# Performance work log

Measured on AMD Instinct MI355X. Metric: run time of the kernel, lower is better.

Reference implementation:

```python
import jax, jax.numpy as jnp
import numpy as np

V, E, H = 32000, 512, 1024  # vocab, embed_dim, hidden_dim
N, T = 32, 256              # batch, seq_len


def setup_inputs() -> dict:
    key = jax.random.key(0)
    ks = jax.random.split(key, 8)
    s = 1.0 / np.sqrt(H)
    return {
        "words": jax.random.randint(ks[0], (N, T), 0, V),
        "hidden_state": jnp.zeros((N, H), jnp.float32),
        "embed_w": jax.random.uniform(ks[1], (V, E), minval=-1.0, maxval=1.0) * 0.1,
        "w_ih": jax.random.uniform(ks[2], (3 * H, E), minval=-s, maxval=s),
        "w_hh": jax.random.uniform(ks[3], (3 * H, H), minval=-s, maxval=s),
        "b_ih": jax.random.uniform(ks[4], (3 * H,), minval=-s, maxval=s),
        "b_hh": jax.random.uniform(ks[5], (3 * H,), minval=-s, maxval=s),
        "emit_w": jax.random.uniform(ks[6], (V, H), minval=-s, maxval=s),
        "emit_b": jnp.zeros((V,), jnp.float32),
    }


def reference(words, hidden_state, embed_w, w_ih, w_hh, b_ih, b_hh, emit_w, emit_b):
    n = words.shape[0]
    emb = embed_w[words]                      # [N, T, E]
    xs = (jnp.swapaxes(emb[:, :-1], 0, 1),    # [T-1, N, E] inputs x_{t-1}
          jnp.swapaxes(words[:, 1:], 0, 1))   # [T-1, N]    targets w_t

    def gru_cell(x, h):
        gi = x @ w_ih.T + b_ih                # [N, 3H]
        gh = h @ w_hh.T + b_hh                # [N, 3H]
        i_r, i_z, i_n = jnp.split(gi, 3, axis=-1)
        h_r, h_z, h_n = jnp.split(gh, 3, axis=-1)
        r = jax.nn.sigmoid(i_r + h_r)
        z = jax.nn.sigmoid(i_z + h_z)
        nn_ = jnp.tanh(i_n + r * h_n)
        return (1.0 - z) * nn_ + z * h

    def step(carry, inp):
        h, acc = carry
        x, w = inp
        h = gru_cell(x, h)
        logits = h @ emit_w.T + emit_b        # [N, V]
        logp = jax.nn.log_softmax(logits, axis=-1)
        ll = jnp.take_along_axis(logp, w[:, None], axis=1)[:, 0]  # [N]
        return (h, acc + ll), None

    acc0 = jnp.zeros((n,), hidden_state.dtype)
    (h_final, word_marginals), _ = jax.lax.scan(step, (hidden_state, acc0), xs)
    return word_marginals, h_final
```

## Files before the change

kernel.cpp:

```cpp
#include <hip/hip_runtime.h>
#include <cstdint>

#define V_    32000
#define E_    512
#define H_    1024
#define N_    32
#define T_    256
#define TS    255
#define NWG_B 64
#define CB_   250
#define RB_   64
#define MROW  8192
#define GI_CB 24

typedef _Float16 f16;
typedef _Float16 half8 __attribute__((ext_vector_type(8)));
typedef float floatx4 __attribute__((ext_vector_type(4)));
typedef unsigned long long u64;


__global__ void prep_emit16(const float* __restrict__ emit_w, f16* __restrict__ out) {
  const int64_t nchunk = (int64_t)V_ * H_ / 8;
  int64_t i = (int64_t)blockIdx.x * blockDim.x + threadIdx.x;
  for (; i < nchunk; i += (int64_t)gridDim.x * blockDim.x) {
    const float4* src = (const float4*)(emit_w + i * 8);
    float4 a = src[0], b = src[1];
    half8 h;
    h[0] = (f16)a.x; h[1] = (f16)a.y; h[2] = (f16)a.z; h[3] = (f16)a.w;
    h[4] = (f16)b.x; h[5] = (f16)b.y; h[6] = (f16)b.z; h[7] = (f16)b.w;
    *(half8*)(out + i * 8) = h;
  }
}

__global__ void prep_whh(const float* __restrict__ w_hh, f16* __restrict__ whh) {
  int idx = blockIdx.x * blockDim.x + threadIdx.x;
  if (idx >= 192 * 32 * 64) return;
  int lane = idx & 63;
  int kt   = (idx >> 6) & 31;
  int jt   = (idx >> 6) >> 5;
  int col  = jt * 16 + (lane & 15);
  int k0   = kt * 32 + (lane >> 4) * 8;
  const float* src = w_hh + (int64_t)col * H_ + k0;
  half8 h;
#pragma unroll
  for (int i = 0; i < 8; ++i) h[i] = (f16)src[i];
  *(half8*)(whh + (int64_t)idx * 8) = h;
}

__global__ void prep_wih16(const float* __restrict__ w_ih, f16* __restrict__ out) {
  int idx = blockIdx.x * blockDim.x + threadIdx.x;
  if (idx >= 3072 * 512 / 8) return;
  const float4* src = (const float4*)(w_ih + (int64_t)idx * 8);
  float4 a = src[0], b = src[1];
  half8 h;
  h[0] = (f16)a.x; h[1] = (f16)a.y; h[2] = (f16)a.z; h[3] = (f16)a.w;
  h[4] = (f16)b.x; h[5] = (f16)b.y; h[6] = (f16)b.z; h[7] = (f16)b.w;
  *(half8*)(out + (int64_t)idx * 8) = h;
}

__global__ void prep_xemb(const int* __restrict__ words, const float* __restrict__ embed_w,
                          f16* __restrict__ xemb) {
  int idx = blockIdx.x * blockDim.x + threadIdx.x;
  if (idx >= TS * N_ * (E_ / 8)) return;
  int u = idx & 63;
  int n = (idx >> 6) & 31;
  int t = idx >> 11;
  int word = words[n * T_ + t];
  const float* src = embed_w + (int64_t)word * E_ + u * 8;
  half8 h;
#pragma unroll
  for (int i = 0; i < 8; ++i) h[i] = (f16)src[i];
  *(half8*)(xemb + (int64_t)(t * N_ + n) * E_ + u * 8) = h;
}

__global__ void prep_init(const float* __restrict__ h0, f16* __restrict__ xh,
                          unsigned* __restrict__ slots) {
  int idx = blockIdx.x * blockDim.x + threadIdx.x;
  if (idx < N_ * H_) {
    f16 v = (f16)h0[idx];
    xh[idx] = v;
    xh[N_ * H_ + idx] = v;
  }
  if (idx < 1024) slots[idx] = 0;
}


#define LDK 72

__launch_bounds__(256, 2)
__global__ void gi_gemm(const f16* __restrict__ xemb, const f16* __restrict__ wih16,
                        f16* __restrict__ gi2) {
  const int cb = blockIdx.x % GI_CB;
  const int rb = blockIdx.x / GI_CB;
  const int tid = threadIdx.x;
  const int w = tid >> 6, lane = tid & 63;
  const int wm = w & 1, wn = w >> 1;
  const int l15 = lane & 15, l4 = lane >> 4;

  __shared__ f16 lA[128 * LDK];
  __shared__ f16 lB[128 * LDK];

  floatx4 acc[4][4];
#pragma unroll
  for (int mt = 0; mt < 4; ++mt)
#pragma unroll
    for (int nt = 0; nt < 4; ++nt) { acc[mt][nt][0] = 0.f; acc[mt][nt][1] = 0.f; acc[mt][nt][2] = 0.f; acc[mt][nt][3] = 0.f; }

  const f16* gA = xemb + (int64_t)rb * 128 * E_;
  const f16* gB = wih16 + (int64_t)cb * 128 * E_;

  for (int kb = 0; kb < 8; ++kb) {
    __syncthreads();
#pragma unroll
    for (int i = 0; i < 4; ++i) {
      int idx = i * 256 + tid;
      int row = idx >> 3, u = idx & 7;
      int64_t goff = (int64_t)row * E_ + kb * 64 + u * 8;
      *(half8*)(lA + row * LDK + u * 8) = *(const half8*)(gA + goff);
      *(half8*)(lB + row * LDK + u * 8) = *(const half8*)(gB + goff);
    }
    __syncthreads();
#pragma unroll
    for (int ks = 0; ks < 2; ++ks) {
      half8 af[4], bf[4];
#pragma unroll
      for (int mt = 0; mt < 4; ++mt)
        af[mt] = *(const half8*)(lA + (wm * 64 + mt * 16 + l15) * LDK + ks * 32 + l4 * 8);
#pragma unroll
      for (int nt = 0; nt < 4; ++nt)
        bf[nt] = *(const half8*)(lB + (wn * 64 + nt * 16 + l15) * LDK + ks * 32 + l4 * 8);
#pragma unroll
      for (int mt = 0; mt < 4; ++mt)
#pragma unroll
        for (int nt = 0; nt < 4; ++nt)
          acc[mt][nt] = __builtin_amdgcn_mfma_f32_16x16x32_f16(af[mt], bf[nt], acc[mt][nt], 0, 0, 0);
    }
  }

#pragma unroll
  for (int mt = 0; mt < 4; ++mt) {
#pragma unroll
    for (int r = 0; r < 4; ++r) {
      int g = rb * 128 + wm * 64 + mt * 16 + l4 * 4 + r;
      if (g < TS * N_) {
        int tt = g >> 5, n = g & 31;
        f16* gb = gi2 + ((int64_t)tt * 3072 + cb * 128 + wn * 64) * 32 + n;
#pragma unroll
        for (int nt = 0; nt < 4; ++nt)
          gb[(nt * 16 + l15) * 32] = (f16)acc[mt][nt][r];
      }
    }
  }
}


__device__ inline u64 aload64(const void* p) {
  return __hip_atomic_load((const u64*)p, __ATOMIC_RELAXED, __HIP_MEMORY_SCOPE_AGENT);
}
__device__ inline unsigned aload32(const void* p) {
  return __hip_atomic_load((const unsigned*)p, __ATOMIC_RELAXED, __HIP_MEMORY_SCOPE_AGENT);
}

__device__ inline void gbar3(unsigned* slots, unsigned tval, int b) {
  __syncthreads();
  if (threadIdx.x == 0) {
    __builtin_amdgcn_s_waitcnt(0);
    __hip_atomic_store(slots + b * 16, tval, __ATOMIC_RELAXED, __HIP_MEMORY_SCOPE_AGENT);
  }
  if (threadIdx.x < 64) {
    unsigned* my = slots + threadIdx.x * 16;
    while (__hip_atomic_load(my, __ATOMIC_RELAXED, __HIP_MEMORY_SCOPE_AGENT) < tval)
      __builtin_amdgcn_s_sleep(1);
  }
  __syncthreads();
}

__launch_bounds__(512, 1)
__global__ void phaseB(const f16* __restrict__ whh, const f16* __restrict__ gi2,
                       f16* __restrict__ xh, const float* __restrict__ b_ih,
                       const float* __restrict__ b_hh, f16* __restrict__ hall,
                       float* __restrict__ out, unsigned* __restrict__ slots) {
  const int b = blockIdx.x;
  const int tid = threadIdx.x;
  const int w = tid >> 6;
  const int lane = tid & 63;
  const int l15 = lane & 15, l4 = lane >> 4;

  __shared__ float part[8][32][49];

  const int n_g = tid & 31;
  const int jl = tid >> 5;
  const int j = b * 16 + jl;
  const float biasr = b_ih[j] + b_hh[j];
  const float biasz = b_ih[H_ + j] + b_hh[H_ + j];
  const float bihn = b_ih[2 * H_ + j];
  const float bhhn = b_hh[2 * H_ + j];

  half8 wf[3][4];
#pragma unroll
  for (int g = 0; g < 3; ++g) {
    int jt = g * 64 + b;
#pragma unroll
    for (int k = 0; k < 4; ++k)
      wf[g][k] = *(const half8*)(whh + (((int64_t)jt * 32 + (w * 4 + k)) * 64 + lane) * 8);
  }

  for (int t = 0; t < TS; ++t) {
    const f16* xh_rd = xh + (t & 1) * (N_ * H_);
    f16* xh_wr = xh + ((t + 1) & 1) * (N_ * H_);

    const f16* gbase = gi2 + (int64_t)t * 3072 * 32 + n_g;
    float gvr = (float)gbase[(int64_t)j * 32];
    float gvz = (float)gbase[(int64_t)(H_ + j) * 32];
    float gvn = (float)gbase[(int64_t)(2 * H_ + j) * 32];
    unsigned hraw = aload32(xh_rd + n_g * H_ + (j & ~1));
    unsigned short hbits = (jl & 1) ? (unsigned short)(hraw >> 16) : (unsigned short)(hraw & 0xffffu);
    float hold = (float)__builtin_bit_cast(f16, hbits);

    floatx4 acc[3][2];
#pragma unroll
    for (int g = 0; g < 3; ++g)
#pragma unroll
      for (int m = 0; m < 2; ++m) { acc[g][m][0] = 0.f; acc[g][m][1] = 0.f; acc[g][m][2] = 0.f; acc[g][m][3] = 0.f; }

    half8 a0[4], a1[4];
#pragma unroll
    for (int k = 0; k < 4; ++k) {
      const f16* base = xh_rd + (w * 4 + k) * 32 + l4 * 8;
      union { half8 h; u64 u[2]; } x0, x1;
      const u64* p0 = (const u64*)(base + (int64_t)l15 * H_);
      const u64* p1 = (const u64*)(base + (int64_t)(l15 + 16) * H_);
      x0.u[0] = aload64(p0); x0.u[1] = aload64(p0 + 1);
      x1.u[0] = aload64(p1); x1.u[1] = aload64(p1 + 1);
      a0[k] = x0.h; a1[k] = x1.h;
    }
#pragma unroll
    for (int k = 0; k < 4; ++k) {
#pragma unroll
      for (int g = 0; g < 3; ++g) {
        acc[g][0] = __builtin_amdgcn_mfma_f32_16x16x32_f16(a0[k], wf[g][k], acc[g][0], 0, 0, 0);
        acc[g][1] = __builtin_amdgcn_mfma_f32_16x16x32_f16(a1[k], wf[g][k], acc[g][1], 0, 0, 0);
      }
    }

#pragma unroll
    for (int g = 0; g < 3; ++g)
#pragma unroll
      for (int m = 0; m < 2; ++m)
#pragma unroll
        for (int r = 0; r < 4; ++r)
          part[w][m * 16 + l4 * 4 + r][g * 16 + l15] = acc[g][m][r];
    __syncthreads();

    float gr = biasr + gvr, gz = biasz + gvz, gin = bihn + gvn, ghn = bhhn;
#pragma unroll
    for (int ww = 0; ww < 8; ++ww) {
      gr += part[ww][n_g][jl];
      gz += part[ww][n_g][16 + jl];
      ghn += part[ww][n_g][32 + jl];
    }
    float rg = 1.f / (1.f + __expf(-gr));
    float zg = 1.f / (1.f + __expf(-gz));
    float nn = tanhf(gin + rg * ghn);
    float hnew = (1.f - zg) * nn + zg * hold;

    unsigned short hb = __builtin_bit_cast(unsigned short, (f16)hnew);
    unsigned other = (unsigned)__shfl_xor((int)(unsigned)hb, 32, 64);
    if (!(jl & 1)) {
      unsigned packed = (unsigned)hb | (other << 16);
      __hip_atomic_store((unsigned*)(xh_wr + n_g * H_ + j), packed,
                         __ATOMIC_RELAXED, __HIP_MEMORY_SCOPE_AGENT);
      *(unsigned*)(hall + ((int64_t)t * N_ + n_g) * H_ + j) = packed;
    }
    if (t == TS - 1) out[32 + n_g * H_ + j] = hnew;

    if (t < TS - 1) gbar3(slots, (unsigned)(t + 1), b);
  }
}


__device__ inline void gload_lds16(const f16* g, f16* l) {
  __builtin_amdgcn_global_load_lds((const __attribute__((address_space(1))) void*)g,
                                   (__attribute__((address_space(3))) void*)l, 16, 0, 0);
}

__launch_bounds__(256, 2)
__global__ void phaseC(const f16* __restrict__ hall, const f16* __restrict__ emit16,
                       const float* __restrict__ emit_b, float* __restrict__ spart) {
  const int wgid = (blockIdx.x & 7) * 2000 + (blockIdx.x >> 3);
  const int cb = wgid >> 6;
  const int rb = wgid & 63;
  const int tid = threadIdx.x;
  const int w = tid >> 6, lane = tid & 63;
  const int wm = w & 1, wn = w >> 1;
  const int l15 = lane & 15, l4 = lane >> 4;

  __shared__ f16 lA[128 * 64];
  __shared__ f16 lB[128 * 64];
  __shared__ float rs[2][128];

  floatx4 acc[4][4];
#pragma unroll
  for (int mt = 0; mt < 4; ++mt)
#pragma unroll
    for (int nt = 0; nt < 4; ++nt) { acc[mt][nt][0] = 0.f; acc[mt][nt][1] = 0.f; acc[mt][nt][2] = 0.f; acc[mt][nt][3] = 0.f; }

  const f16* gA = hall + (int64_t)rb * 128 * H_;
  const f16* gB = emit16 + (int64_t)cb * 128 * H_;

  const int lrow8 = lane >> 3;
  const int sc = (lane & 7) ^ lrow8;
  const int rdx = (l15 & 7) << 3;

  for (int kb = 0; kb < 16; ++kb) {
    __syncthreads();
#pragma unroll
    for (int i = 0; i < 4; ++i) {
      const int r0 = w * 32 + i * 8;
      const int64_t goff = (int64_t)(r0 + lrow8) * H_ + kb * 64 + sc * 8;
      gload_lds16(gA + goff, lA + r0 * 64);
      gload_lds16(gB + goff, lB + r0 * 64);
    }
    __syncthreads();
#pragma unroll
    for (int ks = 0; ks < 2; ++ks) {
      half8 af[4], bf[4];
      const int col = (ks * 32 + l4 * 8) ^ rdx;
#pragma unroll
      for (int mt = 0; mt < 4; ++mt)
        af[mt] = *(const half8*)(lA + (wm * 64 + mt * 16 + l15) * 64 + col);
#pragma unroll
      for (int nt = 0; nt < 4; ++nt)
        bf[nt] = *(const half8*)(lB + (wn * 64 + nt * 16 + l15) * 64 + col);
#pragma unroll
      for (int mt = 0; mt < 4; ++mt)
#pragma unroll
        for (int nt = 0; nt < 4; ++nt)
          acc[mt][nt] = __builtin_amdgcn_mfma_f32_16x16x32_f16(af[mt], bf[nt], acc[mt][nt], 0, 0, 0);
    }
  }

  float eb[4];
#pragma unroll
  for (int nt = 0; nt < 4; ++nt) eb[nt] = emit_b[cb * 128 + wn * 64 + nt * 16 + l15];

#pragma unroll
  for (int mt = 0; mt < 4; ++mt) {
#pragma unroll
    for (int r = 0; r < 4; ++r) {
      float s = 0.f;
#pragma unroll
      for (int nt = 0; nt < 4; ++nt) s += __expf(acc[mt][nt][r] + eb[nt]);
#pragma unroll
      for (int off = 1; off < 16; off <<= 1) s += __shfl_xor(s, off, 64);
      if (l15 == 0) rs[wn][wm * 64 + mt * 16 + l4 * 4 + r] = s;
    }
  }
  __syncthreads();
  if (tid < 128)
    spart[(int64_t)cb * MROW + rb * 128 + tid] = rs[0][tid] + rs[1][tid];
}


__global__ void target_dots(const f16* __restrict__ hall, const f16* __restrict__ emit16,
                            const int* __restrict__ words, const float* __restrict__ emit_b,
                            float* __restrict__ tlog) {
  int r = blockIdx.x * 4 + (threadIdx.x >> 6);
  if (r >= TS * N_) return;
  int lane = threadIdx.x & 63;
  int t = r >> 5, n = r & 31;
  int tgt = words[n * T_ + t + 1];
  const f16* ha = hall + (int64_t)r * H_;
  const f16* ebp = emit16 + (int64_t)tgt * H_;
  float s = 0.f;
#pragma unroll
  for (int c = 0; c < 2; ++c) {
    int k = c * 512 + lane * 8;
    half8 a = *(const half8*)(ha + k);
    half8 b = *(const half8*)(ebp + k);
#pragma unroll
    for (int i = 0; i < 8; ++i) s += (float)a[i] * (float)b[i];
  }
#pragma unroll
  for (int off = 1; off < 64; off <<= 1) s += __shfl_xor(s, off, 64);
  if (lane == 0) tlog[r] = s + emit_b[tgt];
}

__global__ void reduce_lse(const float* __restrict__ spart, const float* __restrict__ tlog,
                           float* __restrict__ lval) {
  int r = blockIdx.x * blockDim.x + threadIdx.x;
  if (r >= TS * N_) return;
  float s = 0.f;
  for (int cb = 0; cb < CB_; ++cb) s += spart[(int64_t)cb * MROW + r];
  lval[r] = tlog[r] - logf(s);
}

__global__ void finalize(const float* __restrict__ lval, float* __restrict__ out) {
  __shared__ float ps[8][32];
  int n = threadIdx.x & 31, sl = threadIdx.x >> 5;
  float s = 0.f;
  for (int i = 0; i < 32; ++i) {
    int t = sl * 32 + i;
    if (t < TS) s += lval[t * N_ + n];
  }
  ps[sl][n] = s;
  __syncthreads();
  if (threadIdx.x < 32) {
    float tot = 0.f;
#pragma unroll
    for (int k = 0; k < 8; ++k) tot += ps[k][threadIdx.x];
    out[threadIdx.x] = tot;
  }
}


extern "C" void kernel_launch(void* const* d_in, const int* in_sizes, int n_in,
                              void* d_out, int out_size, void* d_ws, size_t ws_size,
                              hipStream_t stream) {
  (void)in_sizes; (void)n_in; (void)out_size; (void)ws_size;
  const int*   words   = (const int*)d_in[0];
  const float* h0      = (const float*)d_in[1];
  const float* embed_w = (const float*)d_in[2];
  const float* w_ih    = (const float*)d_in[3];
  const float* w_hh    = (const float*)d_in[4];
  const float* b_ih    = (const float*)d_in[5];
  const float* b_hh    = (const float*)d_in[6];
  const float* emit_w  = (const float*)d_in[7];
  const float* emit_b  = (const float*)d_in[8];
  float* out = (float*)d_out;

  char* ws = (char*)d_ws;
  f16*      big    = (f16*)(ws + 0);
  f16*      gi2    = big;
  f16*      emit16 = big;
  f16*      whh    = (f16*)(ws + 65536000);
  f16*      wih16  = (f16*)(ws + 71827456);
  float*    spart  = (float*)(ws + 71827456);
  f16*      xemb   = (f16*)(ws + 74973184);
  f16*      xh     = (f16*)(ws + 83361792);
  f16*      hall   = (f16*)(ws + 83492864);
  float*    tlog   = (float*)(ws + 100270080);
  float*    lval   = (float*)(ws + 100302720);
  unsigned* slots  = (unsigned*)(ws + 100335360);

  hipLaunchKernelGGL(prep_whh, dim3(1536), dim3(256), 0, stream, w_hh, whh);
  hipLaunchKernelGGL(prep_wih16, dim3(768), dim3(256), 0, stream, w_ih, wih16);
  hipLaunchKernelGGL(prep_xemb, dim3(2040), dim3(256), 0, stream, words, embed_w, xemb);
  hipLaunchKernelGGL(prep_init, dim3(128), dim3(256), 0, stream, h0, xh, slots);
  hipLaunchKernelGGL(gi_gemm, dim3(RB_ * GI_CB), dim3(256), 0, stream, xemb, wih16, gi2);
  hipLaunchKernelGGL(phaseB, dim3(NWG_B), dim3(512), 0, stream, whh, gi2, xh, b_ih, b_hh, hall, out, slots);
  hipLaunchKernelGGL(prep_emit16, dim3(4096), dim3(256), 0, stream, emit_w, emit16);
  hipLaunchKernelGGL(phaseC, dim3(RB_ * CB_), dim3(256), 0, stream, hall, emit16, emit_b, spart);
  hipLaunchKernelGGL(target_dots, dim3((TS * N_ + 3) / 4), dim3(256), 0, stream, hall, emit16, words, emit_b, tlog);
  hipLaunchKernelGGL(reduce_lse, dim3((TS * N_ + 255) / 256), dim3(256), 0, stream, spart, tlog, lval);
  hipLaunchKernelGGL(finalize, dim3(1), dim3(256), 0, stream, lval, out);
}
```

Baseline: 2.594 ms.

## Replace per-block grid barrier with per-wave dataflow flags in GRU recurrence

Removes the full grid barrier between timesteps of the recurrent kernel. Instead, each wave publishes its own flag once its slice of the new hidden state is stored, and each lane spins only on the flag of the producer wave whose hidden-state columns it reads. The partial-sum shared buffer is double-buffered so no trailing __syncthreads is needed, and h_old is kept in a register rather than reloaded. This cuts barrier latency and idle time on the serial critical path, but uses 512 flag slots and relies on relaxed atomics plus waitcnt for ordering, so memory-ordering correctness is a risk.

```diff
diff --git a/kernel.cpp b/kernel.cpp
--- a/kernel.cpp
+++ b/kernel.cpp
@@ -81,7 +81,7 @@
     xh[idx] = v;
     xh[N_ * H_ + idx] = v;
   }
-  if (idx < 1024) slots[idx] = 0;
+  if (idx < 512 * 16) slots[idx] = 0;
 }
 
 
@@ -159,20 +159,6 @@
 }
 __device__ inline unsigned aload32(const void* p) {
   return __hip_atomic_load((const unsigned*)p, __ATOMIC_RELAXED, __HIP_MEMORY_SCOPE_AGENT);
-}
-
-__device__ inline void gbar3(unsigned* slots, unsigned tval, int b) {
-  __syncthreads();
-  if (threadIdx.x == 0) {
-    __builtin_amdgcn_s_waitcnt(0);
-    __hip_atomic_store(slots + b * 16, tval, __ATOMIC_RELAXED, __HIP_MEMORY_SCOPE_AGENT);
-  }
-  if (threadIdx.x < 64) {
-    unsigned* my = slots + threadIdx.x * 16;
-    while (__hip_atomic_load(my, __ATOMIC_RELAXED, __HIP_MEMORY_SCOPE_AGENT) < tval)
-      __builtin_amdgcn_s_sleep(1);
-  }
-  __syncthreads();
 }
 
 __launch_bounds__(512, 1)
@@ -186,7 +172,7 @@
   const int lane = tid & 63;
   const int l15 = lane & 15, l4 = lane >> 4;
 
-  __shared__ float part[8][32][49];
+  __shared__ float part[2][8][32][49];
 
   const int n_g = tid & 31;
   const int jl = tid >> 5;
@@ -205,6 +191,11 @@
       wf[g][k] = *(const half8*)(whh + (((int64_t)jt * 32 + (w * 4 + k)) * 64 + lane) * 8);
   }
 
+  const unsigned* myflag = slots + ((unsigned)(8 * w + (lane >> 3)) * 8 + (lane & 7)) * 16;
+  unsigned* ownflag = slots + ((unsigned)b * 8 + w) * 16;
+
+  float hold = (float)xh[n_g * H_ + j];
+
   for (int t = 0; t < TS; ++t) {
     const f16* xh_rd = xh + (t & 1) * (N_ * H_);
     f16* xh_wr = xh + ((t + 1) & 1) * (N_ * H_);
@@ -213,15 +204,8 @@
     float gvr = (float)gbase[(int64_t)j * 32];
     float gvz = (float)gbase[(int64_t)(H_ + j) * 32];
     float gvn = (float)gbase[(int64_t)(2 * H_ + j) * 32];
-    unsigned hraw = aload32(xh_rd + n_g * H_ + (j & ~1));
-    unsigned short hbits = (jl & 1) ? (unsigned short)(hraw >> 16) : (unsigned short)(hraw & 0xffffu);
-    float hold = (float)__builtin_bit_cast(f16, hbits);
-
-    floatx4 acc[3][2];
-#pragma unroll
-    for (int g = 0; g < 3; ++g)
-#pragma unroll
-      for (int m = 0; m < 2; ++m) { acc[g][m][0] = 0.f; acc[g][m][1] = 0.f; acc[g][m][2] = 0.f; acc[g][m][3] = 0.f; }
+
+    while (aload32(myflag) < (unsigned)t) __builtin_amdgcn_s_sleep(1);
 
     half8 a0[4], a1[4];
 #pragma unroll
@@ -234,6 +218,13 @@
       x1.u[0] = aload64(p1); x1.u[1] = aload64(p1 + 1);
       a0[k] = x0.h; a1[k] = x1.h;
     }
+
+    floatx4 acc[3][2];
+#pragma unroll
+    for (int g = 0; g < 3; ++g)
+#pragma unroll
+      for (int m = 0; m < 2; ++m) { acc[g][m][0] = 0.f; acc[g][m][1] = 0.f; acc[g][m][2] = 0.f; acc[g][m][3] = 0.f; }
+
 #pragma unroll
     for (int k = 0; k < 4; ++k) {
 #pragma unroll
@@ -243,21 +234,22 @@
       }
     }
 
+    float (*pp)[32][49] = part[t & 1];
 #pragma unroll
     for (int g = 0; g < 3; ++g)
 #pragma unroll
       for (int m = 0; m < 2; ++m)
 #pragma unroll
         for (int r = 0; r < 4; ++r)
-          part[w][m * 16 + l4 * 4 + r][g * 16 + l15] = acc[g][m][r];
+          pp[w][m * 16 + l4 * 4 + r][g * 16 + l15] = acc[g][m][r];
     __syncthreads();
 
     float gr = biasr + gvr, gz = biasz + gvz, gin = bihn + gvn, ghn = bhhn;
 #pragma unroll
     for (int ww = 0; ww < 8; ++ww) {
-      gr += part[ww][n_g][jl];
-      gz += part[ww][n_g][16 + jl];
-      ghn += part[ww][n_g][32 + jl];
+      gr += pp[ww][n_g][jl];
+      gz += pp[ww][n_g][16 + jl];
+      ghn += pp[ww][n_g][32 + jl];
     }
     float rg = 1.f / (1.f + __expf(-gr));
     float zg = 1.f / (1.f + __expf(-gz));
@@ -266,15 +258,22 @@
 
     unsigned short hb = __builtin_bit_cast(unsigned short, (f16)hnew);
     unsigned other = (unsigned)__shfl_xor((int)(unsigned)hb, 32, 64);
+    unsigned packed = (unsigned)hb | (other << 16);
     if (!(jl & 1)) {
-      unsigned packed = (unsigned)hb | (other << 16);
       __hip_atomic_store((unsigned*)(xh_wr + n_g * H_ + j), packed,
                          __ATOMIC_RELAXED, __HIP_MEMORY_SCOPE_AGENT);
+    }
+    if (t < TS - 1) {
+      __builtin_amdgcn_s_waitcnt(0);
+      if (lane == 0)
+        __hip_atomic_store(ownflag, (unsigned)(t + 1),
+                           __ATOMIC_RELAXED, __HIP_MEMORY_SCOPE_AGENT);
+    }
+    if (!(jl & 1))
       *(unsigned*)(hall + ((int64_t)t * N_ + n_g) * H_ + j) = packed;
-    }
     if (t == TS - 1) out[32 + n_g * H_ + j] = hnew;
 
-    if (t < TS - 1) gbar3(slots, (unsigned)(t + 1), b);
+    hold = (float)(f16)hnew;
   }
 }
 
```

Measured after the change: 2.685 ms. 1.04x slower.

## Pin recurrent GRU workgroups to one XCD and replace barrier with per-slot flags

Applied to the files above, without the earlier changes.

The recurrent phase now launches 1024 candidate workgroups. Only the 64 that land on the same XCD as the first arrival take slots; the rest exit at once. This keeps all cross-workgroup hidden-state traffic inside one XCD's L2. The all-to-all grid barrier becomes per-producer flags: each wave polls only the 8 producer slots whose hidden slice it reads. The step reads the previous hidden state directly from the hall history, dropping the double-buffered xh copy and its atomic loads. The risks are that too few workgroups may co-reside on a single XCD, which could deadlock, and that the hold value is now carried in registers.

```diff
diff --git a/kernel.cpp b/kernel.cpp
--- a/kernel.cpp
+++ b/kernel.cpp
@@ -8,6 +8,7 @@
 #define T_    256
 #define TS    255
 #define NWG_B 64
+#define CAND_B 1024
 #define CB_   250
 #define RB_   64
 #define MROW  8192
@@ -76,12 +77,8 @@
 __global__ void prep_init(const float* __restrict__ h0, f16* __restrict__ xh,
                           unsigned* __restrict__ slots) {
   int idx = blockIdx.x * blockDim.x + threadIdx.x;
-  if (idx < N_ * H_) {
-    f16 v = (f16)h0[idx];
-    xh[idx] = v;
-    xh[N_ * H_ + idx] = v;
-  }
-  if (idx < 1024) slots[idx] = 0;
+  if (idx < N_ * H_) xh[idx] = (f16)h0[idx];
+  if (idx < 2048) slots[idx] = 0;
 }
 
 
@@ -154,39 +151,43 @@
 }
 
 
-__device__ inline u64 aload64(const void* p) {
-  return __hip_atomic_load((const u64*)p, __ATOMIC_RELAXED, __HIP_MEMORY_SCOPE_AGENT);
-}
 __device__ inline unsigned aload32(const void* p) {
   return __hip_atomic_load((const unsigned*)p, __ATOMIC_RELAXED, __HIP_MEMORY_SCOPE_AGENT);
 }
 
-__device__ inline void gbar3(unsigned* slots, unsigned tval, int b) {
-  __syncthreads();
-  if (threadIdx.x == 0) {
-    __builtin_amdgcn_s_waitcnt(0);
-    __hip_atomic_store(slots + b * 16, tval, __ATOMIC_RELAXED, __HIP_MEMORY_SCOPE_AGENT);
-  }
-  if (threadIdx.x < 64) {
-    unsigned* my = slots + threadIdx.x * 16;
-    while (__hip_atomic_load(my, __ATOMIC_RELAXED, __HIP_MEMORY_SCOPE_AGENT) < tval)
-      __builtin_amdgcn_s_sleep(1);
-  }
-  __syncthreads();
-}
-
 __launch_bounds__(512, 1)
 __global__ void phaseB(const f16* __restrict__ whh, const f16* __restrict__ gi2,
-                       f16* __restrict__ xh, const float* __restrict__ b_ih,
+                       const f16* __restrict__ h0f16, const float* __restrict__ b_ih,
                        const float* __restrict__ b_hh, f16* __restrict__ hall,
                        float* __restrict__ out, unsigned* __restrict__ slots) {
-  const int b = blockIdx.x;
+  __shared__ float part[8][32][49];
+  __shared__ int sh_slot;
+
+  unsigned xcd = __builtin_amdgcn_s_getreg(63508) & 0xFu;
+  if (threadIdx.x == 0) {
+    unsigned* ticket = slots + 1024;
+    unsigned* target = slots + 1028;
+    unsigned* slotc  = slots + 1032;
+    unsigned tk = __hip_atomic_fetch_add(ticket, 1u, __ATOMIC_RELAXED, __HIP_MEMORY_SCOPE_AGENT);
+    if (tk == 0)
+      __hip_atomic_store(target, xcd | 0x100u, __ATOMIC_RELAXED, __HIP_MEMORY_SCOPE_AGENT);
+    unsigned tgt;
+    while ((((tgt = aload32(target))) & 0x100u) == 0) __builtin_amdgcn_s_sleep(1);
+    int myslot = -1;
+    if ((tgt & 0xFu) == xcd) {
+      unsigned s = __hip_atomic_fetch_add(slotc, 1u, __ATOMIC_RELAXED, __HIP_MEMORY_SCOPE_AGENT);
+      if (s < NWG_B) myslot = (int)s;
+    }
+    sh_slot = myslot;
+  }
+  __syncthreads();
+  const int b = sh_slot;
+  if (b < 0) return;
+
   const int tid = threadIdx.x;
   const int w = tid >> 6;
   const int lane = tid & 63;
   const int l15 = lane & 15, l4 = lane >> 4;
-
-  __shared__ float part[8][32][49];
 
   const int n_g = tid & 31;
   const int jl = tid >> 5;
@@ -205,17 +206,30 @@
       wf[g][k] = *(const half8*)(whh + (((int64_t)jt * 32 + (w * 4 + k)) * 64 + lane) * 8);
   }
 
+  unsigned* ownflag = slots + (unsigned)b * 16;
+  const unsigned* pollp = slots + (unsigned)(8 * w + (lane & 7)) * 16;
+
+  float hold = (float)h0f16[n_g * H_ + j];
+
   for (int t = 0; t < TS; ++t) {
-    const f16* xh_rd = xh + (t & 1) * (N_ * H_);
-    f16* xh_wr = xh + ((t + 1) & 1) * (N_ * H_);
-
     const f16* gbase = gi2 + (int64_t)t * 3072 * 32 + n_g;
     float gvr = (float)gbase[(int64_t)j * 32];
     float gvz = (float)gbase[(int64_t)(H_ + j) * 32];
     float gvn = (float)gbase[(int64_t)(2 * H_ + j) * 32];
-    unsigned hraw = aload32(xh_rd + n_g * H_ + (j & ~1));
-    unsigned short hbits = (jl & 1) ? (unsigned short)(hraw >> 16) : (unsigned short)(hraw & 0xffffu);
-    float hold = (float)__builtin_bit_cast(f16, hbits);
+
+    if (lane < 8)
+      while (aload32(pollp) < (unsigned)t) __builtin_amdgcn_s_sleep(1);
+    asm volatile("" ::: "memory");
+
+    const f16* hp = t ? (hall + (int64_t)(t - 1) * N_ * H_) : h0f16;
+
+    half8 a0[4], a1[4];
+#pragma unroll
+    for (int k = 0; k < 4; ++k) {
+      const f16* base = hp + (w * 4 + k) * 32 + l4 * 8;
+      a0[k] = *(const half8*)(base + (int64_t)l15 * H_);
+      a1[k] = *(const half8*)(base + (int64_t)(l15 + 16) * H_);
+    }
 
     floatx4 acc[3][2];
 #pragma unroll
@@ -223,17 +237,6 @@
 #pragma unroll
       for (int m = 0; m < 2; ++m) { acc[g][m][0] = 0.f; acc[g][m][1] = 0.f; acc[g][m][2] = 0.f; acc[g][m][3] = 0.f; }
 
-    half8 a0[4], a1[4];
-#pragma unroll
-    for (int k = 0; k < 4; ++k) {
-      const f16* base = xh_rd + (w * 4 + k) * 32 + l4 * 8;
-      union { half8 h; u64 u[2]; } x0, x1;
-      const u64* p0 = (const u64*)(base + (int64_t)l15 * H_);
-      const u64* p1 = (const u64*)(base + (int64_t)(l15 + 16) * H_);
-      x0.u[0] = aload64(p0); x0.u[1] = aload64(p0 + 1);
-      x1.u[0] = aload64(p1); x1.u[1] = aload64(p1 + 1);
-      a0[k] = x0.h; a1[k] = x1.h;
-    }
 #pragma unroll
     for (int k = 0; k < 4; ++k) {
 #pragma unroll
@@ -266,15 +269,23 @@
 
     unsigned short hb = __builtin_bit_cast(unsigned short, (f16)hnew);
     unsigned other = (unsigned)__shfl_xor((int)(unsigned)hb, 32, 64);
-    if (!(jl & 1)) {
-      unsigned packed = (unsigned)hb | (other << 16);
-      __hip_atomic_store((unsigned*)(xh_wr + n_g * H_ + j), packed,
+    unsigned packed = (unsigned)hb | (other << 16);
+    if (!(jl & 1))
+      __hip_atomic_store((unsigned*)(hall + ((int64_t)t * N_ + n_g) * H_ + j), packed,
                          __ATOMIC_RELAXED, __HIP_MEMORY_SCOPE_AGENT);
-      *(unsigned*)(hall + ((int64_t)t * N_ + n_g) * H_ + j) = packed;
-    }
-    if (t == TS - 1) out[32 + n_g * H_ + j] = hnew;
-
-    if (t < TS - 1) gbar3(slots, (unsigned)(t + 1), b);
+
+    if (t < TS - 1) {
+      __syncthreads();
+      if (tid == 0) {
+        __builtin_amdgcn_s_waitcnt(0);
+        __hip_atomic_store(ownflag, (unsigned)(t + 1),
+                           __ATOMIC_RELAXED, __HIP_MEMORY_SCOPE_AGENT);
+      }
+    } else {
+      out[32 + n_g * H_ + j] = hnew;
+    }
+
+    hold = (float)(f16)hnew;
   }
 }
 
@@ -448,7 +459,7 @@
   hipLaunchKernelGGL(prep_xemb, dim3(2040), dim3(256), 0, stream, words, embed_w, xemb);
   hipLaunchKernelGGL(prep_init, dim3(128), dim3(256), 0, stream, h0, xh, slots);
   hipLaunchKernelGGL(gi_gemm, dim3(RB_ * GI_CB), dim3(256), 0, stream, xemb, wih16, gi2);
-  hipLaunchKernelGGL(phaseB, dim3(NWG_B), dim3(512), 0, stream, whh, gi2, xh, b_ih, b_hh, hall, out, slots);
+  hipLaunchKernelGGL(phaseB, dim3(CAND_B), dim3(512), 0, stream, whh, gi2, xh, b_ih, b_hh, hall, out, slots);
   hipLaunchKernelGGL(prep_emit16, dim3(4096), dim3(256), 0, stream, emit_w, emit16);
   hipLaunchKernelGGL(phaseC, dim3(RB_ * CB_), dim3(256), 0, stream, hall, emit16, emit_b, spart);
   hipLaunchKernelGGL(target_dots, dim3((TS * N_ + 3) / 4), dim3(256), 0, stream, hall, emit16, words, emit_b, tlog);
```

Result: slower. 2.868 ms (+10.6%).

## Fuse GRU recurrence and emission GEMM into one persistent kernel with progress flags

Applied to the files above, without the earlier changes.

Adds a fused persistent kernel in which 64 workgroups run the sequential GRU recurrence while the remaining workgroups pull emission-GEMM tiles from an atomic ticket counter. Each tile waits on a published progress counter until the hidden states for its row block are written. This overlaps the large log-softmax GEMM with the latency-bound recurrence instead of running them back to back. It needs a larger workspace (separate buffers for gi2 and emit16) and falls back to the old path otherwise. It also risks contention, or deadlock if the recurrence workgroups are not all co-resident.

```diff
diff --git a/kernel.cpp b/kernel.cpp
--- a/kernel.cpp
+++ b/kernel.cpp
@@ -12,6 +12,7 @@
 #define RB_   64
 #define MROW  8192
 #define GI_CB 24
+#define FUSED_WS 150486784ULL
 
 typedef _Float16 f16;
 typedef _Float16 half8 __attribute__((ext_vector_type(8)));
@@ -74,14 +75,14 @@
 }
 
 __global__ void prep_init(const float* __restrict__ h0, f16* __restrict__ xh,
-                          unsigned* __restrict__ slots) {
+                          unsigned* __restrict__ slots, int nslots) {
   int idx = blockIdx.x * blockDim.x + threadIdx.x;
   if (idx < N_ * H_) {
     f16 v = (f16)h0[idx];
     xh[idx] = v;
     xh[N_ * H_ + idx] = v;
   }
-  if (idx < 1024) slots[idx] = 0;
+  if (idx < nslots) slots[idx] = 0;
 }
 
 
@@ -160,12 +161,15 @@
 __device__ inline unsigned aload32(const void* p) {
   return __hip_atomic_load((const unsigned*)p, __ATOMIC_RELAXED, __HIP_MEMORY_SCOPE_AGENT);
 }
+__device__ inline void astore32(void* p, unsigned v) {
+  __hip_atomic_store((unsigned*)p, v, __ATOMIC_RELAXED, __HIP_MEMORY_SCOPE_AGENT);
+}
 
 __device__ inline void gbar3(unsigned* slots, unsigned tval, int b) {
   __syncthreads();
   if (threadIdx.x == 0) {
     __builtin_amdgcn_s_waitcnt(0);
-    __hip_atomic_store(slots + b * 16, tval, __ATOMIC_RELAXED, __HIP_MEMORY_SCOPE_AGENT);
+    astore32(slots + b * 16, tval);
   }
   if (threadIdx.x < 64) {
     unsigned* my = slots + threadIdx.x * 16;
@@ -174,6 +178,12 @@
   }
   __syncthreads();
 }
+
+__device__ inline void gload_lds16(const f16* g, f16* l) {
+  __builtin_amdgcn_global_load_lds((const __attribute__((address_space(1))) void*)g,
+                                   (__attribute__((address_space(3))) void*)l, 16, 0, 0);
+}
+
 
 __launch_bounds__(512, 1)
 __global__ void phaseB(const f16* __restrict__ whh, const f16* __restrict__ gi2,
@@ -268,8 +278,7 @@
     unsigned other = (unsigned)__shfl_xor((int)(unsigned)hb, 32, 64);
     if (!(jl & 1)) {
       unsigned packed = (unsigned)hb | (other << 16);
-      __hip_atomic_store((unsigned*)(xh_wr + n_g * H_ + j), packed,
-                         __ATOMIC_RELAXED, __HIP_MEMORY_SCOPE_AGENT);
+      astore32((unsigned*)(xh_wr + n_g * H_ + j), packed);
       *(unsigned*)(hall + ((int64_t)t * N_ + n_g) * H_ + j) = packed;
     }
     if (t == TS - 1) out[32 + n_g * H_ + j] = hnew;
@@ -278,11 +287,6 @@
   }
 }
 
-
-__device__ inline void gload_lds16(const f16* g, f16* l) {
-  __builtin_amdgcn_global_load_lds((const __attribute__((address_space(1))) void*)g,
-                                   (__attribute__((address_space(3))) void*)l, 16, 0, 0);
-}
 
 __launch_bounds__(256, 2)
 __global__ void phaseC(const f16* __restrict__ hall, const f16* __restrict__ emit16,
@@ -359,6 +363,228 @@
   __syncthreads();
   if (tid < 128)
     spart[(int64_t)cb * MROW + rb * 128 + tid] = rs[0][tid] + rs[1][tid];
+}
+
+
+#define FB_TILES 8000
+#define FB_GRID  448
+
+__launch_bounds__(512, 4)
+__global__ void fusedBC(const f16* __restrict__ whh, const f16* __restrict__ gi2,
+                        f16* __restrict__ xh, const float* __restrict__ b_ih,
+                        const float* __restrict__ b_hh, f16* __restrict__ hall,
+                        float* __restrict__ out, unsigned* __restrict__ slots,
+                        const f16* __restrict__ emit16, const float* __restrict__ emit_b,
+                        float* __restrict__ spart) {
+  __shared__ char smem[53248];
+  __shared__ unsigned sclaim;
+  const int bid = blockIdx.x;
+  const int tid = threadIdx.x;
+
+  if (bid < NWG_B) {
+    float (*part)[32][49] = (float (*)[32][49])smem;
+    const int b = bid;
+    const int w = tid >> 6;
+    const int lane = tid & 63;
+    const int l15 = lane & 15, l4 = lane >> 4;
+    const int n_g = tid & 31;
+    const int jl = tid >> 5;
+    const int j = b * 16 + jl;
+    const float biasr = b_ih[j] + b_hh[j];
+    const float biasz = b_ih[H_ + j] + b_hh[H_ + j];
+    const float bihn = b_ih[2 * H_ + j];
+    const float bhhn = b_hh[2 * H_ + j];
+
+    half8 wf[3][4];
+#pragma unroll
+    for (int g = 0; g < 3; ++g) {
+      int jt = g * 64 + b;
+#pragma unroll
+      for (int k = 0; k < 4; ++k)
+        wf[g][k] = *(const half8*)(whh + (((int64_t)jt * 32 + (w * 4 + k)) * 64 + lane) * 8);
+    }
+
+    for (int t = 0; t < TS; ++t) {
+      const f16* xh_rd = xh + (t & 1) * (N_ * H_);
+      f16* xh_wr = xh + ((t + 1) & 1) * (N_ * H_);
+
+      const f16* gbase = gi2 + (int64_t)t * 3072 * 32 + n_g;
+      float gvr = (float)gbase[(int64_t)j * 32];
+      float gvz = (float)gbase[(int64_t)(H_ + j) * 32];
+      float gvn = (float)gbase[(int64_t)(2 * H_ + j) * 32];
+      unsigned hraw = aload32(xh_rd + n_g * H_ + (j & ~1));
+      unsigned short hbits = (jl & 1) ? (unsigned short)(hraw >> 16) : (unsigned short)(hraw & 0xffffu);
+      float hold = (float)__builtin_bit_cast(f16, hbits);
+
+      floatx4 acc[3][2];
+#pragma unroll
+      for (int g = 0; g < 3; ++g)
+#pragma unroll
+        for (int m = 0; m < 2; ++m) { acc[g][m][0] = 0.f; acc[g][m][1] = 0.f; acc[g][m][2] = 0.f; acc[g][m][3] = 0.f; }
+
+      half8 a0[4], a1[4];
+#pragma unroll
+      for (int k = 0; k < 4; ++k) {
+        const f16* base = xh_rd + (w * 4 + k) * 32 + l4 * 8;
+        union { half8 h; u64 u[2]; } x0, x1;
+        const u64* p0 = (const u64*)(base + (int64_t)l15 * H_);
+        const u64* p1 = (const u64*)(base + (int64_t)(l15 + 16) * H_);
+        x0.u[0] = aload64(p0); x0.u[1] = aload64(p0 + 1);
+        x1.u[0] = aload64(p1); x1.u[1] = aload64(p1 + 1);
+        a0[k] = x0.h; a1[k] = x1.h;
+      }
+#pragma unroll
+      for (int k = 0; k < 4; ++k) {
+#pragma unroll
+        for (int g = 0; g < 3; ++g) {
+          acc[g][0] = __builtin_amdgcn_mfma_f32_16x16x32_f16(a0[k], wf[g][k], acc[g][0], 0, 0, 0);
+          acc[g][1] = __builtin_amdgcn_mfma_f32_16x16x32_f16(a1[k], wf[g][k], acc[g][1], 0, 0, 0);
+        }
+      }
+
+#pragma unroll
+      for (int g = 0; g < 3; ++g)
+#pragma unroll
+        for (int m = 0; m < 2; ++m)
+#pragma unroll
+          for (int r = 0; r < 4; ++r)
+            part[w][m * 16 + l4 * 4 + r][g * 16 + l15] = acc[g][m][r];
+      __syncthreads();
+
+      float gr = biasr + gvr, gz = biasz + gvz, gin = bihn + gvn, ghn = bhhn;
+#pragma unroll
+      for (int ww = 0; ww < 8; ++ww) {
+        gr += part[ww][n_g][jl];
+        gz += part[ww][n_g][16 + jl];
+        ghn += part[ww][n_g][32 + jl];
+      }
+      float rg = 1.f / (1.f + __expf(-gr));
+      float zg = 1.f / (1.f + __expf(-gz));
+      float nn = tanhf(gin + rg * ghn);
+      float hnew = (1.f - zg) * nn + zg * hold;
+
+      unsigned short hb = __builtin_bit_cast(unsigned short, (f16)hnew);
+      unsigned other = (unsigned)__shfl_xor((int)(unsigned)hb, 32, 64);
+      if (!(jl & 1)) {
+        unsigned packed = (unsigned)hb | (other << 16);
+        astore32((unsigned*)(xh_wr + n_g * H_ + j), packed);
+        astore32((unsigned*)(hall + ((int64_t)t * N_ + n_g) * H_ + j), packed);
+      }
+      if (t == TS - 1) out[32 + n_g * H_ + j] = hnew;
+
+      if (t < TS - 1) gbar3(slots, (unsigned)(t + 1), b);
+    }
+    __syncthreads();
+    if (tid == 0) {
+      __builtin_amdgcn_s_waitcnt(0);
+      astore32(slots + b * 16, 255u);
+    }
+    return;
+  }
+
+  if (bid == NWG_B) {
+    if (tid >= 64) return;
+    while (true) {
+      unsigned v = aload32(slots + tid * 16);
+#pragma unroll
+      for (int off = 32; off >= 1; off >>= 1) {
+        unsigned o = (unsigned)__shfl_xor((int)v, off, 64);
+        v = v < o ? v : o;
+      }
+      if (tid < 16) astore32(slots + 2048 + tid * 16, v);
+      if (v >= 255u) return;
+      __builtin_amdgcn_s_sleep(8);
+    }
+  }
+
+  {
+    const int w = tid >> 6, lane = tid & 63;
+    const int wm = w & 1, wn = w >> 1;
+    const int l15 = lane & 15, l4 = lane >> 4;
+    const int lrow8 = lane >> 3;
+    const int sc = (lane & 7) ^ lrow8;
+    const int rdx = (l15 & 7) << 3;
+    f16* lA = (f16*)smem;
+    f16* lB = (f16*)(smem + 32768);
+    float* rs = (float*)(smem + 49152);
+    unsigned* ticket = slots + 1024;
+    const unsigned* tline = slots + 2048 + (bid & 15) * 16;
+
+    while (true) {
+      if (tid == 0)
+        sclaim = __hip_atomic_fetch_add(ticket, 1u, __ATOMIC_RELAXED, __HIP_MEMORY_SCOPE_AGENT);
+      __syncthreads();
+      const unsigned c = sclaim;
+      __syncthreads();
+      if (c >= FB_TILES) return;
+      const int rb = (int)(c / 250u);
+      const int cb = (int)(c % 250u);
+      const unsigned thr = (rb == 31) ? 255u : (unsigned)(8 * rb + 8);
+      if (tid == 0)
+        while (aload32(tline) < thr) __builtin_amdgcn_s_sleep(32);
+      __syncthreads();
+      asm volatile("" ::: "memory");
+
+      const f16* gA = hall + (int64_t)rb * 256 * H_;
+      const f16* gB = emit16 + (int64_t)cb * 128 * H_;
+
+      floatx4 acc[8][2];
+#pragma unroll
+      for (int mt = 0; mt < 8; ++mt)
+#pragma unroll
+        for (int nt = 0; nt < 2; ++nt) { acc[mt][nt][0] = 0.f; acc[mt][nt][1] = 0.f; acc[mt][nt][2] = 0.f; acc[mt][nt][3] = 0.f; }
+
+      for (int kb = 0; kb < 16; ++kb) {
+        __syncthreads();
+#pragma unroll
+        for (int i = 0; i < 4; ++i) {
+          const int r0 = w * 32 + i * 8;
+          gload_lds16(gA + (int64_t)(r0 + lrow8) * H_ + kb * 64 + sc * 8, lA + r0 * 64);
+        }
+#pragma unroll
+        for (int i = 0; i < 2; ++i) {
+          const int r0 = w * 16 + i * 8;
+          gload_lds16(gB + (int64_t)(r0 + lrow8) * H_ + kb * 64 + sc * 8, lB + r0 * 64);
+        }
+        __syncthreads();
+#pragma unroll
+        for (int ks = 0; ks < 2; ++ks) {
+          half8 af[8], bf[2];
+          const int col = (ks * 32 + l4 * 8) ^ rdx;
+#pragma unroll
+          for (int mt = 0; mt < 8; ++mt)
+            af[mt] = *(const half8*)(lA + (wm * 128 + mt * 16 + l15) * 64 + col);
+#pragma unroll
+          for (int nt = 0; nt < 2; ++nt)
+            bf[nt] = *(const half8*)(lB + (wn * 32 + nt * 16 + l15) * 64 + col);
+#pragma unroll
+          for (int mt = 0; mt < 8; ++mt)
+#pragma unroll
+            for (int nt = 0; nt < 2; ++nt)
+              acc[mt][nt] = __builtin_amdgcn_mfma_f32_16x16x32_f16(af[mt], bf[nt], acc[mt][nt], 0, 0, 0);
+        }
+      }
+
+      float eb[2];
+#pragma unroll
+      for (int nt = 0; nt < 2; ++nt) eb[nt] = emit_b[cb * 128 + wn * 32 + nt * 16 + l15];
+
+#pragma unroll
+      for (int mt = 0; mt < 8; ++mt) {
+#pragma unroll
+        for (int r = 0; r < 4; ++r) {
+          float s = __expf(acc[mt][0][r] + eb[0]) + __expf(acc[mt][1][r] + eb[1]);
+#pragma unroll
+          for (int off = 1; off < 16; off <<= 1) s += __shfl_xor(s, off, 64);
+          if (l15 == 0) rs[wn * 256 + wm * 128 + mt * 16 + l4 * 4 + r] = s;
+        }
+      }
+      __syncthreads();
+      if (tid < 256)
+        spart[(int64_t)cb * MROW + rb * 256 + tid] =
+            rs[tid] + rs[256 + tid] + rs[512 + tid] + rs[768 + tid];
+    }
+  }
 }
 
 
@@ -417,7 +643,7 @@
 extern "C" void kernel_launch(void* const* d_in, const int* in_sizes, int n_in,
                               void* d_out, int out_size, void* d_ws, size_t ws_size,
                               hipStream_t stream) {
-  (void)in_sizes; (void)n_in; (void)out_size; (void)ws_size;
+  (void)in_sizes; (void)n_in; (void)out_size;
   const int*   words   = (const int*)d_in[0];
   const float* h0      = (const float*)d_in[1];
   const float* embed_w = (const float*)d_in[2];
@@ -430,28 +656,55 @@
   float* out = (float*)d_out;
 
   char* ws = (char*)d_ws;
-  f16*      big    = (f16*)(ws + 0);
-  f16*      gi2    = big;
-  f16*      emit16 = big;
-  f16*      whh    = (f16*)(ws + 65536000);
-  f16*      wih16  = (f16*)(ws + 71827456);
-  float*    spart  = (float*)(ws + 71827456);
-  f16*      xemb   = (f16*)(ws + 74973184);
-  f16*      xh     = (f16*)(ws + 83361792);
-  f16*      hall   = (f16*)(ws + 83492864);
-  float*    tlog   = (float*)(ws + 100270080);
-  float*    lval   = (float*)(ws + 100302720);
-  unsigned* slots  = (unsigned*)(ws + 100335360);
-
-  hipLaunchKernelGGL(prep_whh, dim3(1536), dim3(256), 0, stream, w_hh, whh);
-  hipLaunchKernelGGL(prep_wih16, dim3(768), dim3(256), 0, stream, w_ih, wih16);
-  hipLaunchKernelGGL(prep_xemb, dim3(2040), dim3(256), 0, stream, words, embed_w, xemb);
-  hipLaunchKernelGGL(prep_init, dim3(128), dim3(256), 0, stream, h0, xh, slots);
-  hipLaunchKernelGGL(gi_gemm, dim3(RB_ * GI_CB), dim3(256), 0, stream, xemb, wih16, gi2);
-  hipLaunchKernelGGL(phaseB, dim3(NWG_B), dim3(512), 0, stream, whh, gi2, xh, b_ih, b_hh, hall, out, slots);
-  hipLaunchKernelGGL(prep_emit16, dim3(4096), dim3(256), 0, stream, emit_w, emit16);
-  hipLaunchKernelGGL(phaseC, dim3(RB_ * CB_), dim3(256), 0, stream, hall, emit16, emit_b, spart);
-  hipLaunchKernelGGL(target_dots, dim3((TS * N_ + 3) / 4), dim3(256), 0, stream, hall, emit16, words, emit_b, tlog);
-  hipLaunchKernelGGL(reduce_lse, dim3((TS * N_ + 255) / 256), dim3(256), 0, stream, spart, tlog, lval);
-  hipLaunchKernelGGL(finalize, dim3(1), dim3(256), 0, stream, lval, out);
-}
+
+  if (ws_size >= FUSED_WS) {
+    f16*      emit16 = (f16*)(ws + 0);
+    f16*      gi2    = (f16*)(ws + 65536000);
+    f16*      whh    = (f16*)(ws + 115671040);
+    f16*      xemb   = (f16*)(ws + 121962496);
+    float*    spart  = (float*)(ws + 121962496);
+    f16*      wih16  = (f16*)(ws + 130351104);
+    f16*      xh     = (f16*)(ws + 133496832);
+    f16*      hall   = (f16*)(ws + 133627904);
+    float*    tlog   = (float*)(ws + 150405120);
+    float*    lval   = (float*)(ws + 150437760);
+    unsigned* slots  = (unsigned*)(ws + 150470400);
+
+    hipLaunchKernelGGL(prep_whh, dim3(1536), dim3(256), 0, stream, w_hh, whh);
+    hipLaunchKernelGGL(prep_wih16, dim3(768), dim3(256), 0, stream, w_ih, wih16);
+    hipLaunchKernelGGL(prep_xemb, dim3(2040), dim3(256), 0, stream, words, embed_w, xemb);
+    hipLaunchKernelGGL(prep_init, dim3(128), dim3(256), 0, stream, h0, xh, slots, 4096);
+    hipLaunchKernelGGL(prep_emit16, dim3(4096), dim3(256), 0, stream, emit_w, emit16);
+    hipLaunchKernelGGL(gi_gemm, dim3(RB_ * GI_CB), dim3(256), 0, stream, xemb, wih16, gi2);
+    hipLaunchKernelGGL(fusedBC, dim3(FB_GRID), dim3(512), 0, stream,
+                       whh, gi2, xh, b_ih, b_hh, hall, out, slots, emit16, emit_b, spart);
+    hipLaunchKernelGGL(target_dots, dim3((TS * N_ + 3) / 4), dim3(256), 0, stream, hall, emit16, words, emit_b, tlog);
+    hipLaunchKernelGGL(reduce_lse, dim3((TS * N_ + 255) / 256), dim3(256), 0, stream, spart, tlog, lval);
+    hipLaunchKernelGGL(finalize, dim3(1), dim3(256), 0, stream, lval, out);
+  } else {
+    f16*      big    = (f16*)(ws + 0);
+    f16*      gi2    = big;
+    f16*      emit16 = big;
+    f16*      whh    = (f16*)(ws + 65536000);
+    f16*      wih16  = (f16*)(ws + 71827456);
+    float*    spart  = (float*)(ws + 71827456);
+    f16*      xemb   = (f16*)(ws + 74973184);
+    f16*      xh     = (f16*)(ws + 83361792);
+    f16*      hall   = (f16*)(ws + 83492864);
+    float*    tlog   = (float*)(ws + 100270080);
+    float*    lval   = (float*)(ws + 100302720);
+    unsigned* slots  = (unsigned*)(ws + 100335360);
+
+    hipLaunchKernelGGL(prep_whh, dim3(1536), dim3(256), 0, stream, w_hh, whh);
+    hipLaunchKernelGGL(prep_wih16, dim3(768), dim3(256), 0, stream, w_ih, wih16);
+    hipLaunchKernelGGL(prep_xemb, dim3(2040), dim3(256), 0, stream, words, embed_w, xemb);
+    hipLaunchKernelGGL(prep_init, dim3(128), dim3(256), 0, stream, h0, xh, slots, 1024);
+    hipLaunchKernelGGL(gi_gemm, dim3(RB_ * GI_CB), dim3(256), 0, stream, xemb, wih16, gi2);
+    hipLaunchKernelGGL(phaseB, dim3(NWG_B), dim3(512), 0, stream, whh, gi2, xh, b_ih, b_hh, hall, out, slots);
+    hipLaunchKernelGGL(prep_emit16, dim3(4096), dim3(256), 0, stream, emit_w, emit16);
+    hipLaunchKernelGGL(phaseC, dim3(RB_ * CB_), dim3(256), 0, stream, hall, emit16, emit_b, spart);
+    hipLaunchKernelGGL(target_dots, dim3((TS * N_ + 3) / 4), dim3(256), 0, stream, hall, emit16, words, emit_b, tlog);
+    hipLaunchKernelGGL(reduce_lse, dim3((TS * N_ + 255) / 256), dim3(256), 0, stream, spart, tlog, lval);
+    hipLaunchKernelGGL(finalize, dim3(1), dim3(256), 0, stream, lval, out);
+  }
+}
```

Result: faster. 2.331 ms (-10.1%).
